# Kernel tuning notes

Hardware: AMD Instinct MI355X
Metric: run time of the kernel (lower is better)

Reference implementation:

```python
import jax, jax.numpy as jnp
import numpy as np

B, IC, OC, K, L = 64, 2, 32, 5, 65536
FS = 50000000.0
J_MAX = 16  # upper bound on resampled kernel length (alpha >= ~0.4 here)
# PERTURB_ORDER = ['CFO','SCALE','GAIN','SHIFT','CHIRP'] -> columns 0..4


def setup_inputs() -> dict:
    key = jax.random.key(0)
    k1, k2, k3, k4 = jax.random.split(key, 4)
    x = jax.random.normal(k1, (B, IC, 1, L), dtype=jnp.float32)
    z = jax.random.randint(k2, (B, 5), 0, 2).astype(jnp.int32)  # perturbation on/off gates
    u = jax.random.uniform(k3, (B, 5), dtype=jnp.float32)
    s = jnp.stack([
        -800.0 + 1600.0 * u[:, 0],   # CFO  (Hz)
        0.8 + 0.5 * u[:, 1],         # SCALE alpha in [0.8, 1.3]
        0.7 + 0.6 * u[:, 2],         # GAIN rho in [0.7, 1.3]
        u[:, 3],                     # SHIFT (unused on kernels)
        -2000.0 + 4000.0 * u[:, 4],  # CHIRP slope
    ], axis=1)
    # kaiming_uniform_(a=0.2, 'relu'... torch uses leaky_relu gain formula with a)
    fan_in = IC * 1 * K
    gain = float(np.sqrt(2.0 / (1.0 + 0.2 ** 2)))
    bound = gain * float(np.sqrt(3.0 / fan_in))
    w0 = jax.random.uniform(k4, (OC, IC, 1, K), minval=-bound, maxval=bound, dtype=jnp.float32)
    return {"x": x, "z": z, "s": s, "w0": w0}


def _resample_matrix(new_W):
    """[K,K] matrix = upsample(new_W->K) @ downsample(K->new_W), linear, align_corners=False."""
    nWf = new_W.astype(jnp.float32)
    # stage 1: K -> new_W  (rows j >= new_W are zero / padded)
    j = jnp.arange(J_MAX, dtype=jnp.float32)
    valid = (j < nWf).astype(jnp.float32)
    src1 = jnp.maximum((j + 0.5) * K / nWf - 0.5, 0.0)
    i0 = jnp.floor(src1).astype(jnp.int32)
    i1 = jnp.minimum(i0 + 1, K - 1)
    lam1 = src1 - i0.astype(jnp.float32)
    eyeK = jnp.eye(K, dtype=jnp.float32)
    W1 = valid[:, None] * ((1.0 - lam1)[:, None] * eyeK[i0] + lam1[:, None] * eyeK[i1])  # [J_MAX,K]
    # stage 2: new_W -> K
    i = jnp.arange(K, dtype=jnp.float32)
    src2 = jnp.maximum((i + 0.5) * nWf / K - 0.5, 0.0)
    j0 = jnp.floor(src2).astype(jnp.int32)
    j1 = jnp.minimum(j0 + 1, new_W - 1)
    lam2 = src2 - j0.astype(jnp.float32)
    eyeJ = jnp.eye(J_MAX, dtype=jnp.float32)
    W2 = (1.0 - lam2)[:, None] * eyeJ[j0] + lam2[:, None] * eyeJ[j1]  # [K,J_MAX]
    return W2 @ W1  # [K,K]


def _rot_iq(w, phi):
    """w: [B,OC,IC,K], phi: [B,K] -> rotate I/Q channels by per-tap phase."""
    I, Q = w[:, :, 0, :], w[:, :, 1, :]
    c = jnp.cos(phi)[:, None, :]
    sn = jnp.sin(phi)[:, None, :]
    return jnp.stack([I * c - Q * sn, I * sn + Q * c], axis=2)


def _forward(x, z, s, w0):
    Bx = x.shape[0]
    Lx = x.shape[-1]
    def param(col, neutral):
        m = z[:, col] > 0
        return jnp.where(m, jnp.nan_to_num(s[:, col]), jnp.float32(neutral))
    alpha = param(1, 1.0)   # coef_scale=1: 1 + 1*(alpha-1) = alpha
    f0 = param(0, 0.0)
    a = param(4, 0.0)
    rho = param(2, 1.0)
    theta = jnp.zeros_like(rho)
    w = jnp.broadcast_to(w0[None, :, :, 0, :], (Bx, OC, IC, K))  # [B,OC,IC,K]
    # SCALE: per-sample down/up linear resample as a [K,K] operator
    new_W = jnp.clip(jnp.round(K / jnp.maximum(alpha, 0.001)), 1, J_MAX).astype(jnp.int32)
    M = jax.vmap(_resample_matrix)(new_W)  # [B,K,K]
    w = jnp.einsum('bxy,boiy->boix', M, w)
    # CFO then CHIRP phase mixing
    n = jnp.arange(K, dtype=jnp.float32)
    w = _rot_iq(w, 2.0 * jnp.pi * f0[:, None] * n / FS)
    w = _rot_iq(w, jnp.pi * a[:, None] * (n / FS) ** 2)
    # GAIN: theta=0 rotation + rho scaling
    cg, sg = jnp.cos(theta)[:, None, None], jnp.sin(theta)[:, None, None]
    I, Q = w[:, :, 0, :], w[:, :, 1, :]
    w = jnp.stack([cg * I - sg * Q, sg * I + cg * Q], axis=2)
    w = rho[:, None, None, None] * w
    # grouped conv: groups = B
    xG = x.reshape(1, Bx * IC, 1, Lx)
    wG = w.reshape(Bx * OC, IC, 1, K)
    yG = jax.lax.conv_general_dilated(
        xG, wG, window_strides=(1, 1), padding=((0, 0), (K // 2, K // 2)),
        dimension_numbers=('NCHW', 'OIHW', 'NCHW'), feature_group_count=Bx)
    return yG.reshape(Bx, OC, 1, Lx)


def reference(x, z, s, w0):
    return _forward(x, z, s, w0)
```

## Files before the change

### kernel.cpp

```cpp
#include <hip/hip_runtime.h>
#include <math.h>
#include <float.h>

constexpr int Bn  = 64;
constexpr int ICn = 2;
constexpr int OCn = 32;
constexpr int Kn  = 5;
constexpr int Ln  = 65536;
constexpr float FSc = 50000000.0f;
constexpr int JMAXn = 16;

constexpr int TPB   = 256;
constexpr int CHUNK = 16384;
constexpr int NCH   = Ln / CHUNK;
constexpr int ITERS = CHUNK / (TPB * 4);

typedef float f32x4 __attribute__((ext_vector_type(4)));

__global__ __launch_bounds__(64) void wgen_kernel(const int* __restrict__ z,
                                                  const float* __restrict__ s,
                                                  const float* __restrict__ w0,
                                                  float* __restrict__ w) {
    const int b  = blockIdx.x;
    const int oc = threadIdx.x;
    if (oc >= OCn) return;

    float pv[5];
#pragma unroll
    for (int c = 0; c < 5; ++c) {
        float v = s[b * 5 + c];
        if (isnan(v)) v = 0.0f;
        else if (isinf(v)) v = (v > 0.0f) ? FLT_MAX : -FLT_MAX;
        pv[c] = v;
    }
    const float neutral[5] = {0.0f, 1.0f, 1.0f, 0.0f, 0.0f};
#pragma unroll
    for (int c = 0; c < 5; ++c) {
        if (!(z[b * 5 + c] > 0)) pv[c] = neutral[c];
    }
    const float f0    = pv[0];
    const float alpha = pv[1];
    const float rho   = pv[2];
    const float a     = pv[4];

    float nw = rintf(5.0f / fmaxf(alpha, 0.001f));
    int new_W = (int)nw;
    if (new_W < 1) new_W = 1;
    if (new_W > JMAXn) new_W = JMAXn;
    const float nWf = (float)new_W;

    float M[Kn][Kn];
#pragma unroll
    for (int xi = 0; xi < Kn; ++xi)
#pragma unroll
        for (int y = 0; y < Kn; ++y) M[xi][y] = 0.0f;

#pragma unroll
    for (int xi = 0; xi < Kn; ++xi) {
        const float src2 = fmaxf((xi + 0.5f) * nWf / 5.0f - 0.5f, 0.0f);
        const int   j0   = (int)floorf(src2);
        const int   j1   = min(j0 + 1, new_W - 1);
        const float lam2 = src2 - (float)j0;
        const int   jj[2] = {j0, j1};
        const float cf[2] = {1.0f - lam2, lam2};
#pragma unroll
        for (int t = 0; t < 2; ++t) {
            const int   j  = jj[t];
            const float cc = cf[t];
            const float src1 = fmaxf((j + 0.5f) * 5.0f / nWf - 0.5f, 0.0f);
            const int   i0   = (int)floorf(src1);
            const int   i1   = min(i0 + 1, Kn - 1);
            const float lam1 = src1 - (float)i0;
#pragma unroll
            for (int y = 0; y < Kn; ++y) {
                const float e = ((y == i0) ? (1.0f - lam1) : 0.0f) +
                                ((y == i1) ? lam1 : 0.0f);
                M[xi][y] += cc * e;
            }
        }
    }

    const float* w0b = w0 + oc * (ICn * Kn);
    float wI[Kn], wQ[Kn];
#pragma unroll
    for (int xi = 0; xi < Kn; ++xi) {
        float aI = 0.0f, aQ = 0.0f;
#pragma unroll
        for (int y = 0; y < Kn; ++y) {
            aI += M[xi][y] * w0b[y];
            aQ += M[xi][y] * w0b[Kn + y];
        }
        wI[xi] = aI;
        wQ[xi] = aQ;
    }

    const float c2pi = (float)(2.0 * M_PI);
    const float cpi  = (float)M_PI;
#pragma unroll
    for (int n = 0; n < Kn; ++n) {
        const float nf  = (float)n;
        const float ph1 = ((c2pi * f0) * nf) / FSc;
        const float c1 = cosf(ph1), s1 = sinf(ph1);
        float I = wI[n], Q = wQ[n];
        float I2 = I * c1 - Q * s1;
        float Q2 = I * s1 + Q * c1;
        const float t   = nf / FSc;
        const float ph2 = (cpi * a) * (t * t);
        const float c2 = cosf(ph2), s2 = sinf(ph2);
        float I3 = I2 * c2 - Q2 * s2;
        float Q3 = I2 * s2 + Q2 * c2;
        wI[n] = rho * I3;
        wQ[n] = rho * Q3;
    }

    float* wb = w + (b * OCn + oc) * (ICn * Kn);
#pragma unroll
    for (int k = 0; k < Kn; ++k) {
        wb[k]      = wI[k];
        wb[Kn + k] = wQ[k];
    }
}

__global__ __launch_bounds__(TPB) void conv_kernel(const float* __restrict__ x,
                                                   const float* __restrict__ w,
                                                   float* __restrict__ y) {
    const int blk   = blockIdx.x;
    const int chunk = blk & (NCH - 1);
    const int oc    = (blk >> 2) & (OCn - 1);
    const int b     = blk >> 7;

    const float* wo = w + (size_t)(b * OCn + oc) * (ICn * Kn);
    float wv[ICn * Kn];
#pragma unroll
    for (int i = 0; i < ICn * Kn; ++i) wv[i] = wo[i];

    const float* x0 = x + (size_t)b * (ICn * Ln);
    const float* x1 = x0 + Ln;
    float* yo = y + ((size_t)(b * OCn + oc)) * Ln + chunk * CHUNK;

    const int l0base = chunk * CHUNK + (int)threadIdx.x * 4;

#pragma unroll 2
    for (int it = 0; it < ITERS; ++it) {
        const int l0 = l0base + it * (TPB * 4);
        float xa[12], xc[12];
        if (l0 >= 4 && l0 + 8 <= Ln) {
#pragma unroll
            for (int q = 0; q < 3; ++q) {
                const float4 va = *reinterpret_cast<const float4*>(x0 + l0 - 4 + 4 * q);
                const float4 vb = *reinterpret_cast<const float4*>(x1 + l0 - 4 + 4 * q);
                xa[4 * q + 0] = va.x; xa[4 * q + 1] = va.y;
                xa[4 * q + 2] = va.z; xa[4 * q + 3] = va.w;
                xc[4 * q + 0] = vb.x; xc[4 * q + 1] = vb.y;
                xc[4 * q + 2] = vb.z; xc[4 * q + 3] = vb.w;
            }
        } else {
#pragma unroll
            for (int m = 0; m < 12; ++m) {
                const int g = l0 - 4 + m;
                const bool ok = (g >= 0 && g < Ln);
                xa[m] = ok ? x0[g] : 0.0f;
                xc[m] = ok ? x1[g] : 0.0f;
            }
        }

        float a0 = 0.0f, a1 = 0.0f, a2 = 0.0f, a3 = 0.0f;
#pragma unroll
        for (int k = 0; k < Kn; ++k) {
            const float wA = wv[k];
            const float wB = wv[Kn + k];
            a0 = fmaf(wA, xa[k + 2], a0); a0 = fmaf(wB, xc[k + 2], a0);
            a1 = fmaf(wA, xa[k + 3], a1); a1 = fmaf(wB, xc[k + 3], a1);
            a2 = fmaf(wA, xa[k + 4], a2); a2 = fmaf(wB, xc[k + 4], a2);
            a3 = fmaf(wA, xa[k + 5], a3); a3 = fmaf(wB, xc[k + 5], a3);
        }

        f32x4 v = {a0, a1, a2, a3};
        __builtin_nontemporal_store(
            v, reinterpret_cast<f32x4*>(yo + it * (TPB * 4) + (int)threadIdx.x * 4));
    }
}

extern "C" void kernel_launch(void* const* d_in, const int* in_sizes, int n_in,
                              void* d_out, int out_size, void* d_ws, size_t ws_size,
                              hipStream_t stream) {
    const float* x  = (const float*)d_in[0];
    const int*   z  = (const int*)d_in[1];
    const float* s  = (const float*)d_in[2];
    const float* w0 = (const float*)d_in[3];
    float* y = (float*)d_out;
    float* w = (float*)d_ws;

    hipLaunchKernelGGL(wgen_kernel, dim3(Bn), dim3(64), 0, stream, z, s, w0, w);
    hipLaunchKernelGGL(conv_kernel, dim3(Bn * OCn * NCH), dim3(TPB), 0, stream, x, w, y);
}
```

Measured before the change: 131.7 us.

## Remap conv threads to (oc, position) and loop over batch inside each thread

Each thread now owns four output positions for one output channel and iterates over all 64 batch samples, instead of each block covering a 16K chunk of one (batch, oc) row. The output channel is made wave-uniform with readfirstlane so weight loads become scalar, and the boundary check is hoisted out of the loop. The grid shrinks to 2048 blocks, each thread writing outputs strided by a batch slice. The aim is to cut per-block setup and weight reloads, at the cost of less total parallelism and more scattered write streams.

```diff
diff --git a/kernel.cpp b/kernel.cpp
--- a/kernel.cpp
+++ b/kernel.cpp
@@ -10,10 +10,9 @@
 constexpr float FSc = 50000000.0f;
 constexpr int JMAXn = 16;
 
-constexpr int TPB   = 256;
-constexpr int CHUNK = 16384;
-constexpr int NCH   = Ln / CHUNK;
-constexpr int ITERS = CHUNK / (TPB * 4);
+constexpr int TPB    = 256;
+constexpr int NBLK   = 2048;
+constexpr int SLICE  = OCn * Ln;
 
 typedef float f32x4 __attribute__((ext_vector_type(4)));
 
@@ -124,27 +123,28 @@
 __global__ __launch_bounds__(TPB) void conv_kernel(const float* __restrict__ x,
                                                    const float* __restrict__ w,
                                                    float* __restrict__ y) {
-    const int blk   = blockIdx.x;
-    const int chunk = blk & (NCH - 1);
-    const int oc    = (blk >> 2) & (OCn - 1);
-    const int b     = blk >> 7;
+    const int t  = (int)blockIdx.x * TPB + (int)threadIdx.x;
+    const int f0 = t * 4;
+    const int oc = f0 >> 16;
+    const int l0 = f0 & (Ln - 1);
+    const int oc_u = __builtin_amdgcn_readfirstlane(oc);
 
-    const float* wo = w + (size_t)(b * OCn + oc) * (ICn * Kn);
-    float wv[ICn * Kn];
+    const bool fast = (l0 >= 4) && (l0 + 8 <= Ln);
+
+    const float* xrow = x;
+    float*       yrow = y + f0;
+
+    for (int b = 0; b < Bn; ++b) {
+        const float* wo = w + (size_t)(b * OCn + oc_u) * (ICn * Kn);
+        float wv[ICn * Kn];
 #pragma unroll
-    for (int i = 0; i < ICn * Kn; ++i) wv[i] = wo[i];
+        for (int i = 0; i < ICn * Kn; ++i) wv[i] = wo[i];
 
-    const float* x0 = x + (size_t)b * (ICn * Ln);
-    const float* x1 = x0 + Ln;
-    float* yo = y + ((size_t)(b * OCn + oc)) * Ln + chunk * CHUNK;
+        const float* x0 = xrow;
+        const float* x1 = xrow + Ln;
 
-    const int l0base = chunk * CHUNK + (int)threadIdx.x * 4;
-
-#pragma unroll 2
-    for (int it = 0; it < ITERS; ++it) {
-        const int l0 = l0base + it * (TPB * 4);
         float xa[12], xc[12];
-        if (l0 >= 4 && l0 + 8 <= Ln) {
+        if (fast) {
 #pragma unroll
             for (int q = 0; q < 3; ++q) {
                 const float4 va = *reinterpret_cast<const float4*>(x0 + l0 - 4 + 4 * q);
@@ -176,8 +176,10 @@
         }
 
         f32x4 v = {a0, a1, a2, a3};
-        __builtin_nontemporal_store(
-            v, reinterpret_cast<f32x4*>(yo + it * (TPB * 4) + (int)threadIdx.x * 4));
+        __builtin_nontemporal_store(v, reinterpret_cast<f32x4*>(yrow));
+
+        xrow += ICn * Ln;
+        yrow += SLICE;
     }
 }
 
@@ -192,5 +194,5 @@
     float* w = (float*)d_ws;
 
     hipLaunchKernelGGL(wgen_kernel, dim3(Bn), dim3(64), 0, stream, z, s, w0, w);
-    hipLaunchKernelGGL(conv_kernel, dim3(Bn * OCn * NCH), dim3(TPB), 0, stream, x, w, y);
+    hipLaunchKernelGGL(conv_kernel, dim3(NBLK), dim3(TPB), 0, stream, x, w, y);
 }
```

New measurement: 147.0 us. 1.12x slower.

## Stage input chunk with halo in LDS and shrink chunk size

Applied to the files above, without the earlier changes.

Each block now cooperatively loads its 4096-sample input chunk for both channels, plus halo, into shared memory, then computes outputs from LDS instead of issuing overlapping global float4 loads. The chunk size drops from 16384 to 4096, which quadruples the block count and removes the boundary branch from the inner loop. The main cost is still writing the 537 MB output, so the gain from cutting redundant global reads may be small, and it adds a barrier plus LDS traffic per block.

```diff
diff --git a/kernel.cpp b/kernel.cpp
--- a/kernel.cpp
+++ b/kernel.cpp
@@ -11,9 +11,10 @@
 constexpr int JMAXn = 16;
 
 constexpr int TPB   = 256;
-constexpr int CHUNK = 16384;
+constexpr int CHUNK = 4096;
 constexpr int NCH   = Ln / CHUNK;
-constexpr int ITERS = CHUNK / (TPB * 4);
+constexpr int ROW   = 4 + CHUNK + 8;
+constexpr int GPT   = CHUNK / (TPB * 4);
 
 typedef float f32x4 __attribute__((ext_vector_type(4)));
 
@@ -124,44 +125,55 @@
 __global__ __launch_bounds__(TPB) void conv_kernel(const float* __restrict__ x,
                                                    const float* __restrict__ w,
                                                    float* __restrict__ y) {
+    __shared__ float lds[2 * ROW];
+
     const int blk   = blockIdx.x;
     const int chunk = blk & (NCH - 1);
-    const int oc    = (blk >> 2) & (OCn - 1);
-    const int b     = blk >> 7;
+    const int oc    = (blk >> 4) & (OCn - 1);
+    const int b     = blk >> 9;
+    const int tid   = (int)threadIdx.x;
+    const int cs    = chunk * CHUNK;
+
+    const float* xb = x + (size_t)b * (ICn * Ln);
+
+#pragma unroll
+    for (int q = 0; q < 8; ++q) {
+        const int f4  = q * TPB + tid;
+        const int ic  = f4 >> 10;
+        const int off = (f4 & 1023) * 4;
+        const float4 v = *reinterpret_cast<const float4*>(xb + ic * Ln + cs + off);
+        *reinterpret_cast<float4*>(&lds[ic * ROW + 4 + off]) = v;
+    }
+    if (tid < 24) {
+        const int ic = tid / 12;
+        const int m  = tid % 12;
+        int gl, li;
+        if (m < 4) { gl = cs - 4 + m;     li = m; }
+        else       { gl = cs + CHUNK + (m - 4); li = 4 + CHUNK + (m - 4); }
+        lds[ic * ROW + li] = (gl >= 0 && gl < Ln) ? xb[ic * Ln + gl] : 0.0f;
+    }
 
     const float* wo = w + (size_t)(b * OCn + oc) * (ICn * Kn);
     float wv[ICn * Kn];
 #pragma unroll
     for (int i = 0; i < ICn * Kn; ++i) wv[i] = wo[i];
 
-    const float* x0 = x + (size_t)b * (ICn * Ln);
-    const float* x1 = x0 + Ln;
-    float* yo = y + ((size_t)(b * OCn + oc)) * Ln + chunk * CHUNK;
-
-    const int l0base = chunk * CHUNK + (int)threadIdx.x * 4;
+    __syncthreads();
+
+    float* yo = y + ((size_t)(b * OCn + oc)) * Ln + cs;
 
 #pragma unroll 2
-    for (int it = 0; it < ITERS; ++it) {
-        const int l0 = l0base + it * (TPB * 4);
+    for (int g = 0; g < GPT; ++g) {
+        const int ll = g * (TPB * 4) + tid * 4;
         float xa[12], xc[12];
-        if (l0 >= 4 && l0 + 8 <= Ln) {
-#pragma unroll
-            for (int q = 0; q < 3; ++q) {
-                const float4 va = *reinterpret_cast<const float4*>(x0 + l0 - 4 + 4 * q);
-                const float4 vb = *reinterpret_cast<const float4*>(x1 + l0 - 4 + 4 * q);
-                xa[4 * q + 0] = va.x; xa[4 * q + 1] = va.y;
-                xa[4 * q + 2] = va.z; xa[4 * q + 3] = va.w;
-                xc[4 * q + 0] = vb.x; xc[4 * q + 1] = vb.y;
-                xc[4 * q + 2] = vb.z; xc[4 * q + 3] = vb.w;
-            }
-        } else {
-#pragma unroll
-            for (int m = 0; m < 12; ++m) {
-                const int g = l0 - 4 + m;
-                const bool ok = (g >= 0 && g < Ln);
-                xa[m] = ok ? x0[g] : 0.0f;
-                xc[m] = ok ? x1[g] : 0.0f;
-            }
+#pragma unroll
+        for (int q = 0; q < 3; ++q) {
+            const float4 va = *reinterpret_cast<const float4*>(&lds[ll + 4 * q]);
+            const float4 vb = *reinterpret_cast<const float4*>(&lds[ROW + ll + 4 * q]);
+            xa[4 * q + 0] = va.x; xa[4 * q + 1] = va.y;
+            xa[4 * q + 2] = va.z; xa[4 * q + 3] = va.w;
+            xc[4 * q + 0] = vb.x; xc[4 * q + 1] = vb.y;
+            xc[4 * q + 2] = vb.z; xc[4 * q + 3] = vb.w;
         }
 
         float a0 = 0.0f, a1 = 0.0f, a2 = 0.0f, a3 = 0.0f;
@@ -176,8 +188,7 @@
         }
 
         f32x4 v = {a0, a1, a2, a3};
-        __builtin_nontemporal_store(
-            v, reinterpret_cast<f32x4*>(yo + it * (TPB * 4) + (int)threadIdx.x * 4));
+        __builtin_nontemporal_store(v, reinterpret_cast<f32x4*>(yo + ll));
     }
 }
 
```

Measured after the change: 147.3 us. 1.12x slower.
